# Optimization experiments

Hardware: AMD Instinct MI355X
Metric: run time of the kernel (lower is better)

Reference implementation:

```python
import jax, jax.numpy as jnp
import numpy as np

HIDDEN = 1024
HEADS = 16
HEAD_DIM = HIDDEN // HEADS
ROPE_BASE = 10000.0


def rope_cos_sin(seq_len, head_dim, dtype=jnp.float32):
    inv_freq = 1.0 / (ROPE_BASE ** (jnp.arange(0, head_dim, 2, dtype=jnp.float32) / head_dim))
    t = jnp.arange(seq_len, dtype=jnp.float32)
    freqs = jnp.einsum('i,j->ij', t, inv_freq)          # [L, head_dim/2]
    emb = jnp.concatenate([freqs, freqs], axis=-1)       # [L, head_dim]
    return emb.astype(dtype), jnp.cos(emb).astype(dtype), jnp.sin(emb).astype(dtype)


def rotate_half(x):
    half = x.shape[-1] // 2
    return jnp.concatenate([-x[..., half:], x[..., :half]], axis=-1)


def setup_inputs() -> dict:
    key = jax.random.key(0)
    kx, kq, kk, kv, ko = jax.random.split(key, 5)
    B, L = 4, 2048
    scale = 1.0 / np.sqrt(HIDDEN)
    x = jax.random.normal(kx, (B, L, HIDDEN), dtype=jnp.float32)
    Wq = jax.random.normal(kq, (HIDDEN, HIDDEN), dtype=jnp.float32) * scale
    Wk = jax.random.normal(kk, (HIDDEN, HIDDEN), dtype=jnp.float32) * scale
    Wv = jax.random.normal(kv, (HIDDEN, HIDDEN), dtype=jnp.float32) * scale
    Wo = jax.random.normal(ko, (HIDDEN, HIDDEN), dtype=jnp.float32) * scale
    return {"x": x, "Wq": Wq, "Wk": Wk, "Wv": Wv, "Wo": Wo}


def reference(x, Wq, Wk, Wv, Wo):
    B, L, D = x.shape
    H, Hd = HEADS, HEAD_DIM
    # projections (nn.Linear: y = x @ W.T; weights here stored already as [out,in])
    q = (x @ Wq.T).reshape(B, L, H, Hd).transpose(0, 2, 1, 3)  # [B,H,L,Hd]
    k = (x @ Wk.T).reshape(B, L, H, Hd).transpose(0, 2, 1, 3)
    v = (x @ Wv.T).reshape(B, L, H, Hd).transpose(0, 2, 1, 3)
    _, cos, sin = rope_cos_sin(L, Hd, x.dtype)                  # [L, Hd]
    cos = cos[None, None, :, :]
    sin = sin[None, None, :, :]
    q = q * cos + rotate_half(q) * sin
    k = k * cos + rotate_half(k) * sin
    scores = jnp.einsum('bhqd,bhkd->bhqk', q, k) / np.sqrt(Hd)  # [B,H,L,L]
    attn = jax.nn.softmax(scores, axis=-1)
    out = jnp.einsum('bhqk,bhkd->bhqd', attn, v)                # [B,H,L,Hd]
    out = out.transpose(0, 2, 1, 3).reshape(B, L, D)
    return out @ Wo.T
```

## Files before the change

### kernel.cpp

```cpp
#include <hip/hip_runtime.h>
#include <math.h>

#define BB 4
#define LL 2048
#define DD 1024
#define HH 16
#define HD 64
#define BL (BB*LL)

typedef __attribute__((ext_vector_type(8))) short bf16x8;
typedef __attribute__((ext_vector_type(4))) short bf16x4;
typedef __attribute__((ext_vector_type(4))) float f32x4;

__device__ inline short f2bf(float f) {
    union { float f; unsigned u; } v; v.f = f;
    unsigned r = v.u + 0x7fffu + ((v.u >> 16) & 1u);
    return (short)(r >> 16);
}

__device__ inline unsigned pk_bf16(float a, float b) {
    union { float f; unsigned u; } x, y; x.f = a; y.f = b;
#if __has_builtin(__builtin_amdgcn_perm)
    return __builtin_amdgcn_perm(y.u, x.u, 0x07060302u);
#else
    return (x.u >> 16) | (y.u & 0xffff0000u);
#endif
}

__device__ inline float exp2x(float x) {
#if __has_builtin(__builtin_amdgcn_exp2f)
    return __builtin_amdgcn_exp2f(x);
#else
    return exp2f(x);
#endif
}

__device__ inline void gload_lds16(const void* g, void* l) {
    __builtin_amdgcn_global_load_lds(
        (const __attribute__((address_space(1))) unsigned int*)g,
        (__attribute__((address_space(3))) unsigned int*)l, 16, 0, 0);
}

__global__ __launch_bounds__(256) void cast_kernel(
    const float* __restrict__ in, short* __restrict__ out, int n)
{
    int i = (blockIdx.x * 256 + threadIdx.x) * 8;
    float4 a = *(const float4*)(in + i);
    float4 b = *(const float4*)(in + i + 4);
    bf16x8 o;
    o[0]=f2bf(a.x); o[1]=f2bf(a.y); o[2]=f2bf(a.z); o[3]=f2bf(a.w);
    o[4]=f2bf(b.x); o[5]=f2bf(b.y); o[6]=f2bf(b.z); o[7]=f2bf(b.w);
    *(bf16x8*)(out + i) = o;
}

__global__ __launch_bounds__(256) void cast4_kernel(
    const float* __restrict__ w0, const float* __restrict__ w1,
    const float* __restrict__ w2, const float* __restrict__ w3,
    short* __restrict__ out)
{
    const int nw_blocks = (DD*DD) / 2048;
    int sel = blockIdx.x / nw_blocks;
    int blk = blockIdx.x % nw_blocks;
    const float* in = (sel == 0) ? w0 : (sel == 1) ? w1 : (sel == 2) ? w2 : w3;
    int i = (blk * 256 + threadIdx.x) * 8;
    float4 a = *(const float4*)(in + i);
    float4 b = *(const float4*)(in + i + 4);
    bf16x8 o;
    o[0]=f2bf(a.x); o[1]=f2bf(a.y); o[2]=f2bf(a.z); o[3]=f2bf(a.w);
    o[4]=f2bf(b.x); o[5]=f2bf(b.y); o[6]=f2bf(b.z); o[7]=f2bf(b.w);
    *(bf16x8*)(out + (size_t)sel * DD * DD + i) = o;
}

__global__ __launch_bounds__(256) void rope_tab_kernel(float2* __restrict__ tab)
{
    int idx = blockIdx.x * 256 + threadIdx.x;
    int lq = idx >> 5, f = idx & 31;
    float inv = __expf((float)f * (-9.210340371976184f / 32.0f));
    float s, c;
    sincosf((float)lq * inv, &s, &c);
    tab[idx] = make_float2(c, s);
}

__device__ inline void gemm_bt_128(const short* __restrict__ A,
                                   const short* __restrict__ B,
                                   short* Ash, short* Bsh,
                                   int i0, int n0, f32x4 (&acc)[4][4])
{
    const int t  = threadIdx.x;
    const int w  = t >> 6;
    const int l  = t & 63;
    const int g  = (t >> 4) & 3;
    const int ln = t & 15;
    const int rh = (w >> 1) * 64;
    const int ch = (w & 1) * 64;
    const int srow = w * 8 + (l >> 3);
    const int skol = (l & 7) * 8;

    for (int k0 = 0; k0 < DD; k0 += 64) {
        __syncthreads();
        const short* ga = A + (size_t)(i0 + srow) * DD + k0 + skol;
        const short* gb = B + (size_t)(n0 + srow) * DD + k0 + skol;
        short* la = Ash + w * 512;
        short* lb = Bsh + w * 512;
        #pragma unroll
        for (int j = 0; j < 4; ++j) {
            gload_lds16(ga + j * 32 * DD, la + j * 2048);
            gload_lds16(gb + j * 32 * DD, lb + j * 2048);
        }
        __syncthreads();

        #pragma unroll
        for (int kk = 0; kk < 2; ++kk) {
            bf16x8 af[4], bfr[4];
            #pragma unroll
            for (int mi = 0; mi < 4; ++mi)
                af[mi] = *(const bf16x8*)(Ash + (rh + mi*16 + ln)*64 + kk*32 + 8*g);
            #pragma unroll
            for (int nj = 0; nj < 4; ++nj)
                bfr[nj] = *(const bf16x8*)(Bsh + (ch + nj*16 + ln)*64 + kk*32 + 8*g);
            #pragma unroll
            for (int mi = 0; mi < 4; ++mi)
                #pragma unroll
                for (int nj = 0; nj < 4; ++nj)
                    acc[mi][nj] = __builtin_amdgcn_mfma_f32_16x16x32_bf16(
                        af[mi], bfr[nj], acc[mi][nj], 0, 0, 0);
        }
    }
}

__global__ __launch_bounds__(256) void qkv_mfma_kernel(
    const short* __restrict__ xb, const short* __restrict__ Wqb,
    const short* __restrict__ Wkb, const short* __restrict__ Wvb,
    const float2* __restrict__ rope_tab,
    short* __restrict__ Qo, short* __restrict__ Ko, short* __restrict__ Vo)
{
    __shared__ short Ash[128*64];
    __shared__ short Bsh[128*64];

    const int gid = blockIdx.x;
    const int r8  = gid & 7;
    const int u   = gid >> 3;
    const int i_idx = r8 * 8 + (u & 7);
    const int nz  = u >> 3;
    const int n_idx = nz & 7;
    const int z   = nz >> 3;

    const short* Wm = (z == 0) ? Wqb : ((z == 1) ? Wkb : Wvb);
    const int i0 = i_idx * 128;
    const int n0 = n_idx * 128;

    f32x4 acc[4][4];
    #pragma unroll
    for (int mi = 0; mi < 4; ++mi)
        #pragma unroll
        for (int nj = 0; nj < 4; ++nj) acc[mi][nj] = (f32x4){0.f,0.f,0.f,0.f};

    gemm_bt_128(xb, Wm, Ash, Bsh, i0, n0, acc);

    const int t  = threadIdx.x;
    const int w  = t >> 6;
    const int g  = (t >> 4) & 3;
    const int ln = t & 15;
    const int rh = (w >> 1) * 64;

    if (z == 2) {
        short* buf = Ash;
        const int b = i0 >> 11, l0 = i0 & (LL - 1);
        const int d = t >> 2;
        const int c = t & 3;
        #pragma unroll
        for (int hp = 0; hp < 2; ++hp) {
            __syncthreads();
            if ((w & 1) == hp) {
                #pragma unroll
                for (int nj = 0; nj < 4; ++nj)
                    #pragma unroll
                    for (int mi = 0; mi < 4; ++mi)
                        #pragma unroll
                        for (int r = 0; r < 4; ++r)
                            buf[(nj*16 + ln)*136 + rh + mi*16 + 4*g + r]
                                = f2bf(acc[mi][nj][r]);
            }
            __syncthreads();
            short* dst = Vo + ((size_t)((b*HH + n_idx*2 + hp)*HD + d)) * LL + l0;
            #pragma unroll
            for (int j = 0; j < 4; ++j) {
                const short* src = buf + d*136 + c*8 + j*32;
                bf16x4 lo = *(const bf16x4*)(src);
                bf16x4 hi = *(const bf16x4*)(src + 4);
                const int tb = (j >> 1) * 64;
                const int hb = j & 1;
                const int aa = c >> 1;
                const int g0 = (c & 1) * 2;
                *(bf16x4*)(dst + tb + g0*16       + hb*8 + aa*4) = lo;
                *(bf16x4*)(dst + tb + (g0+1)*16   + hb*8 + aa*4) = hi;
            }
        }
    } else {
        const int h = n_idx * 2 + (w & 1);
        short* Om = (z == 0) ? Qo : Ko;
        const float sc = (z == 0) ? 0.180336880111112f : 1.0f;
        #pragma unroll
        for (int mi = 0; mi < 4; ++mi)
            #pragma unroll
            for (int r = 0; r < 4; ++r) {
                int i = i0 + rh + mi*16 + 4*g + r;
                int b = i >> 11, lq = i & (LL - 1);
                float2 cs0 = rope_tab[lq*32 + ln];
                float2 cs1 = rope_tab[lq*32 + ln + 16];
                float r0 = (acc[mi][0][r]*cs0.x - acc[mi][2][r]*cs0.y) * sc;
                float r2 = (acc[mi][2][r]*cs0.x + acc[mi][0][r]*cs0.y) * sc;
                float r1 = (acc[mi][1][r]*cs1.x - acc[mi][3][r]*cs1.y) * sc;
                float r3 = (acc[mi][3][r]*cs1.x + acc[mi][1][r]*cs1.y) * sc;
                size_t base = ((size_t)(b*HH + h) * LL + lq) * HD;
                Om[base + ln     ] = f2bf(r0);
                Om[base + ln + 16] = f2bf(r1);
                Om[base + ln + 32] = f2bf(r2);
                Om[base + ln + 48] = f2bf(r3);
            }
    }
}

__global__ __launch_bounds__(256) void attn_kernel(
    const short* __restrict__ Q, const short* __restrict__ K,
    const short* __restrict__ VT, short* __restrict__ AO)
{
    __shared__ short Ksh[64*72];
    __shared__ short VTs[64*72];

    const int t  = threadIdx.x;
    const int w  = t >> 6;
    const int l  = t & 63;
    const int g  = l >> 4;
    const int ln = l & 15;

    const int bh = blockIdx.x;
    const int q0 = blockIdx.y * 128;
    const short* Qb  = Q  + ((size_t)bh * LL + q0 + w*32) * HD;
    const short* Kb  = K  + (size_t)bh * LL * HD;
    const short* VTb = VT + (size_t)bh * HD * LL;

    bf16x8 qb[2][2];
    #pragma unroll
    for (int qi = 0; qi < 2; ++qi) {
        qb[qi][0] = *(const bf16x8*)(Qb + (size_t)(qi*16 + ln)*HD + 8*g);
        qb[qi][1] = *(const bf16x8*)(Qb + (size_t)(qi*16 + ln)*HD + 32 + 8*g);
    }

    const bf16x8 ONES = { (short)0x3F80, (short)0x3F80, (short)0x3F80, (short)0x3F80,
                          (short)0x3F80, (short)0x3F80, (short)0x3F80, (short)0x3F80 };

    f32x4 O[2][4];
    #pragma unroll
    for (int qi = 0; qi < 2; ++qi)
        #pragma unroll
        for (int db = 0; db < 4; ++db) O[qi][db] = (f32x4){0.f,0.f,0.f,0.f};
    f32x4 lsum[2];
    lsum[0] = (f32x4){0.f,0.f,0.f,0.f};
    lsum[1] = (f32x4){0.f,0.f,0.f,0.f};

    const int sr = t >> 2;
    const int sc = (t & 3) << 4;

    for (int kt = 0; kt < LL; kt += 64) {
        bf16x8 k0 = *(const bf16x8*)(Kb  + (size_t)(kt + sr)*HD + sc);
        bf16x8 k1 = *(const bf16x8*)(Kb  + (size_t)(kt + sr)*HD + sc + 8);
        bf16x8 v0 = *(const bf16x8*)(VTb + (size_t)sr*LL + kt + sc);
        bf16x8 v1 = *(const bf16x8*)(VTb + (size_t)sr*LL + kt + sc + 8);
        __syncthreads();
        *(bf16x8*)(Ksh + sr*72 + sc)     = k0;
        *(bf16x8*)(Ksh + sr*72 + sc + 8) = k1;
        *(bf16x8*)(VTs + sr*72 + sc)     = v0;
        *(bf16x8*)(VTs + sr*72 + sc + 8) = v1;
        __syncthreads();

        unsigned pf[2][4][2];
        #pragma unroll
        for (int kb = 0; kb < 4; ++kb) {
            bf16x8 ka0 = *(const bf16x8*)(Ksh + (kb*16 + ln)*72 + 8*g);
            bf16x8 ka1 = *(const bf16x8*)(Ksh + (kb*16 + ln)*72 + 32 + 8*g);
            #pragma unroll
            for (int qi = 0; qi < 2; ++qi) {
                f32x4 S = (f32x4){0.f,0.f,0.f,0.f};
                S = __builtin_amdgcn_mfma_f32_16x16x32_bf16(ka0, qb[qi][0], S, 0, 0, 0);
                S = __builtin_amdgcn_mfma_f32_16x16x32_bf16(ka1, qb[qi][1], S, 0, 0, 0);
                float p0 = exp2x(S[0]), p1 = exp2x(S[1]);
                float p2 = exp2x(S[2]), p3 = exp2x(S[3]);
                pf[qi][kb][0] = pk_bf16(p0, p1);
                pf[qi][kb][1] = pk_bf16(p2, p3);
            }
        }

        bf16x8 pa[2][2];
        #pragma unroll
        for (int qi = 0; qi < 2; ++qi)
            #pragma unroll
            for (int hb = 0; hb < 2; ++hb) {
                union { unsigned u[4]; bf16x8 v; } a;
                a.u[0] = pf[qi][2*hb][0];   a.u[1] = pf[qi][2*hb][1];
                a.u[2] = pf[qi][2*hb+1][0]; a.u[3] = pf[qi][2*hb+1][1];
                pa[qi][hb] = a.v;
            }

        #pragma unroll
        for (int hb = 0; hb < 2; ++hb) {
            lsum[0] = __builtin_amdgcn_mfma_f32_16x16x32_bf16(pa[0][hb], ONES, lsum[0], 0, 0, 0);
            lsum[1] = __builtin_amdgcn_mfma_f32_16x16x32_bf16(pa[1][hb], ONES, lsum[1], 0, 0, 0);
        }

        #pragma unroll
        for (int hb = 0; hb < 2; ++hb) {
            #pragma unroll
            for (int db = 0; db < 4; ++db) {
                bf16x8 vf = *(const bf16x8*)(VTs + (db*16 + ln)*72 + 16*g + 8*hb);
                O[0][db] = __builtin_amdgcn_mfma_f32_16x16x32_bf16(pa[0][hb], vf, O[0][db], 0, 0, 0);
                O[1][db] = __builtin_amdgcn_mfma_f32_16x16x32_bf16(pa[1][hb], vf, O[1][db], 0, 0, 0);
            }
        }
    }

    const int b = bh >> 4, h = bh & 15;
    #pragma unroll
    for (int qi = 0; qi < 2; ++qi) {
        #pragma unroll
        for (int r = 0; r < 4; ++r) {
            float inv = 1.0f / lsum[qi][r];
            int q = q0 + w*32 + qi*16 + 4*g + r;
            size_t base = ((size_t)(b*LL + q)) * DD + h*HD;
            #pragma unroll
            for (int db = 0; db < 4; ++db)
                AO[base + db*16 + ln] = f2bf(O[qi][db][r] * inv);
        }
    }
}

__global__ __launch_bounds__(256) void oproj_mfma_kernel(
    const short* __restrict__ A, const short* __restrict__ Wob,
    float* __restrict__ out)
{
    __shared__ short Ash[128*64];
    __shared__ short Bsh[128*64];

    const int gid = blockIdx.x;
    const int r8  = gid & 7;
    const int u   = gid >> 3;
    const int i_idx = r8 * 8 + (u & 7);
    const int n_idx = u >> 3;
    const int i0 = i_idx * 128;
    const int n0 = n_idx * 128;

    f32x4 acc[4][4];
    #pragma unroll
    for (int mi = 0; mi < 4; ++mi)
        #pragma unroll
        for (int nj = 0; nj < 4; ++nj) acc[mi][nj] = (f32x4){0.f,0.f,0.f,0.f};

    gemm_bt_128(A, Wob, Ash, Bsh, i0, n0, acc);

    const int t  = threadIdx.x;
    const int w  = t >> 6;
    const int g  = (t >> 4) & 3;
    const int ln = t & 15;
    const int rh = (w >> 1) * 64;
    const int ch = (w & 1) * 64;

    #pragma unroll
    for (int mi = 0; mi < 4; ++mi)
        #pragma unroll
        for (int r = 0; r < 4; ++r) {
            size_t base = (size_t)(i0 + rh + mi*16 + 4*g + r) * DD + n0 + ch;
            #pragma unroll
            for (int nj = 0; nj < 4; ++nj)
                out[base + nj*16 + ln] = acc[mi][nj][r];
        }
}

extern "C" void kernel_launch(void* const* d_in, const int* in_sizes, int n_in,
                              void* d_out, int out_size, void* d_ws, size_t ws_size,
                              hipStream_t stream) {
    const float* x  = (const float*)d_in[0];
    const float* Wq = (const float*)d_in[1];
    const float* Wk = (const float*)d_in[2];
    const float* Wv = (const float*)d_in[3];
    const float* Wo = (const float*)d_in[4];
    float* out = (float*)d_out;

    const size_t n_x = (size_t)BL * DD;
    const size_t n_w = (size_t)DD * DD;
    short* xb  = (short*)d_ws;
    short* Wqb = xb  + n_x;
    short* Wkb = Wqb + n_w;
    short* Wvb = Wkb + n_w;
    short* Wob = Wvb + n_w;
    short* Q   = Wob + n_w;
    short* K   = Q   + n_x;
    short* VTg = K   + n_x;
    short* AOb = VTg + n_x;
    float2* tab = (float2*)(AOb + n_x);

    rope_tab_kernel<<<256, 256, 0, stream>>>(tab);
    cast_kernel<<<n_x/2048, 256, 0, stream>>>(x, xb, (int)n_x);
    cast4_kernel<<<4*(n_w/2048), 256, 0, stream>>>(Wq, Wk, Wv, Wo, Wqb);

    qkv_mfma_kernel<<<1536, 256, 0, stream>>>(xb, Wqb, Wkb, Wvb, tab, Q, K, VTg);

    dim3 g2(BB*HH, LL/128);
    attn_kernel<<<g2, 256, 0, stream>>>(Q, K, VTg, AOb);

    oproj_mfma_kernel<<<512, 256, 0, stream>>>(AOb, Wob, out);
}
```

Measured before the change: 272.9 us.

## Double-buffer LDS tiles in QKV and output projection GEMMs

Replaces the single-buffer GEMM main loop with a two-stage ping-pong LDS pipeline, so global-to-LDS loads for the next K slice are issued before the MFMA work on the current slice. This is meant to hide load latency behind compute and halve the number of barrier pairs per K step. It doubles LDS use per block to 64 KB, which may cut occupancy.

```diff
diff --git a/kernel.cpp b/kernel.cpp
--- a/kernel.cpp
+++ b/kernel.cpp
@@ -81,10 +81,45 @@
     tab[idx] = make_float2(c, s);
 }
 
-__device__ inline void gemm_bt_128(const short* __restrict__ A,
-                                   const short* __restrict__ B,
-                                   short* Ash, short* Bsh,
-                                   int i0, int n0, f32x4 (&acc)[4][4])
+__device__ inline void stage8(const short* __restrict__ A,
+                              const short* __restrict__ B,
+                              short* la, short* lb,
+                              int i0, int n0, int k0, int srow, int skol)
+{
+    const short* ga = A + (size_t)(i0 + srow) * DD + k0 + skol;
+    const short* gb = B + (size_t)(n0 + srow) * DD + k0 + skol;
+    #pragma unroll
+    for (int j = 0; j < 4; ++j) {
+        gload_lds16(ga + j * 32 * DD, la + j * 2048);
+        gload_lds16(gb + j * 32 * DD, lb + j * 2048);
+    }
+}
+
+__device__ inline void comp64(const short* Ab, const short* Bb,
+                              int rh, int ch, int g, int ln, f32x4 (&acc)[4][4])
+{
+    #pragma unroll
+    for (int kk = 0; kk < 2; ++kk) {
+        bf16x8 af[4], bfr[4];
+        #pragma unroll
+        for (int mi = 0; mi < 4; ++mi)
+            af[mi] = *(const bf16x8*)(Ab + (rh + mi*16 + ln)*64 + kk*32 + 8*g);
+        #pragma unroll
+        for (int nj = 0; nj < 4; ++nj)
+            bfr[nj] = *(const bf16x8*)(Bb + (ch + nj*16 + ln)*64 + kk*32 + 8*g);
+        #pragma unroll
+        for (int mi = 0; mi < 4; ++mi)
+            #pragma unroll
+            for (int nj = 0; nj < 4; ++nj)
+                acc[mi][nj] = __builtin_amdgcn_mfma_f32_16x16x32_bf16(
+                    af[mi], bfr[nj], acc[mi][nj], 0, 0, 0);
+    }
+}
+
+__device__ inline void gemm_bt_128_db(const short* __restrict__ A,
+                                      const short* __restrict__ B,
+                                      short* S,
+                                      int i0, int n0, f32x4 (&acc)[4][4])
 {
     const int t  = threadIdx.x;
     const int w  = t >> 6;
@@ -96,35 +131,20 @@
     const int srow = w * 8 + (l >> 3);
     const int skol = (l & 7) * 8;
 
-    for (int k0 = 0; k0 < DD; k0 += 64) {
+    short* A0 = S;          short* A1 = S + 8192;
+    short* B0 = S + 16384;  short* B1 = S + 24576;
+    short* la0 = A0 + w*512; short* la1 = A1 + w*512;
+    short* lb0 = B0 + w*512; short* lb1 = B1 + w*512;
+
+    stage8(A, B, la0, lb0, i0, n0, 0, srow, skol);
+    for (int k0 = 0; k0 < DD; k0 += 128) {
         __syncthreads();
-        const short* ga = A + (size_t)(i0 + srow) * DD + k0 + skol;
-        const short* gb = B + (size_t)(n0 + srow) * DD + k0 + skol;
-        short* la = Ash + w * 512;
-        short* lb = Bsh + w * 512;
-        #pragma unroll
-        for (int j = 0; j < 4; ++j) {
-            gload_lds16(ga + j * 32 * DD, la + j * 2048);
-            gload_lds16(gb + j * 32 * DD, lb + j * 2048);
-        }
+        stage8(A, B, la1, lb1, i0, n0, k0 + 64, srow, skol);
+        comp64(A0, B0, rh, ch, g, ln, acc);
         __syncthreads();
-
-        #pragma unroll
-        for (int kk = 0; kk < 2; ++kk) {
-            bf16x8 af[4], bfr[4];
-            #pragma unroll
-            for (int mi = 0; mi < 4; ++mi)
-                af[mi] = *(const bf16x8*)(Ash + (rh + mi*16 + ln)*64 + kk*32 + 8*g);
-            #pragma unroll
-            for (int nj = 0; nj < 4; ++nj)
-                bfr[nj] = *(const bf16x8*)(Bsh + (ch + nj*16 + ln)*64 + kk*32 + 8*g);
-            #pragma unroll
-            for (int mi = 0; mi < 4; ++mi)
-                #pragma unroll
-                for (int nj = 0; nj < 4; ++nj)
-                    acc[mi][nj] = __builtin_amdgcn_mfma_f32_16x16x32_bf16(
-                        af[mi], bfr[nj], acc[mi][nj], 0, 0, 0);
-        }
+        if (k0 + 128 < DD)
+            stage8(A, B, la0, lb0, i0, n0, k0 + 128, srow, skol);
+        comp64(A1, B1, rh, ch, g, ln, acc);
     }
 }
 
@@ -134,8 +154,7 @@
     const float2* __restrict__ rope_tab,
     short* __restrict__ Qo, short* __restrict__ Ko, short* __restrict__ Vo)
 {
-    __shared__ short Ash[128*64];
-    __shared__ short Bsh[128*64];
+    __shared__ short S[32768];
 
     const int gid = blockIdx.x;
     const int r8  = gid & 7;
@@ -155,7 +174,7 @@
         #pragma unroll
         for (int nj = 0; nj < 4; ++nj) acc[mi][nj] = (f32x4){0.f,0.f,0.f,0.f};
 
-    gemm_bt_128(xb, Wm, Ash, Bsh, i0, n0, acc);
+    gemm_bt_128_db(xb, Wm, S, i0, n0, acc);
 
     const int t  = threadIdx.x;
     const int w  = t >> 6;
@@ -164,7 +183,7 @@
     const int rh = (w >> 1) * 64;
 
     if (z == 2) {
-        short* buf = Ash;
+        short* buf = S;
         const int b = i0 >> 11, l0 = i0 & (LL - 1);
         const int d = t >> 2;
         const int c = t & 3;
@@ -338,8 +357,7 @@
     const short* __restrict__ A, const short* __restrict__ Wob,
     float* __restrict__ out)
 {
-    __shared__ short Ash[128*64];
-    __shared__ short Bsh[128*64];
+    __shared__ short S[32768];
 
     const int gid = blockIdx.x;
     const int r8  = gid & 7;
@@ -355,7 +373,7 @@
         #pragma unroll
         for (int nj = 0; nj < 4; ++nj) acc[mi][nj] = (f32x4){0.f,0.f,0.f,0.f};
 
-    gemm_bt_128(A, Wob, Ash, Bsh, i0, n0, acc);
+    gemm_bt_128_db(A, Wob, S, i0, n0, acc);
 
     const int t  = threadIdx.x;
     const int w  = t >> 6;
```

Result: slower. 296.7 us (+8.7%).
